# Kernel tuning notes

Measured on AMD Instinct MI355X. Metric: run time of the kernel, lower is better.

## Reference

```python
import jax, jax.numpy as jnp
import numpy as np

N = 50000      # nodes
E = 800000     # edges
P = 100000     # pos/neg candidate edges
IN = 128       # input feat dim
H, D = 2, 64   # heads, out_feats per head
HD = H * D     # 128
NEG_SLOPE = 0.2


def setup_inputs() -> dict:
    key = jax.random.key(0)
    ks = jax.random.split(key, 18)
    def gn(k, shape, fan_in):
        return jax.random.normal(k, shape, jnp.float32) * (1.0 / np.sqrt(fan_in))
    return {
        "x": jax.random.normal(ks[0], (N, IN), jnp.float32),
        "src": jax.random.randint(ks[1], (E,), 0, N),
        "dst": jax.random.randint(ks[2], (E,), 0, N),
        "pos_src": jax.random.randint(ks[3], (P,), 0, N),
        "pos_dst": jax.random.randint(ks[4], (P,), 0, N),
        "neg_src": jax.random.randint(ks[5], (P,), 0, N),
        "neg_dst": jax.random.randint(ks[6], (P,), 0, N),
        "W0": gn(ks[7], (IN, HD), IN),
        "attn0": gn(ks[8], (H, D), D),
        "W1": gn(ks[9], (HD, HD), HD),
        "attn1": gn(ks[10], (H, D), D),
        "Wp1": gn(ks[11], (HD, D), HD),
        "bp1": jnp.zeros((D,), jnp.float32),
        "Wp2": gn(ks[12], (D, D), D),
        "bp2": jnp.zeros((D,), jnp.float32),
        "Wp3": gn(ks[13], (D, 1), D),
        "bp3": jnp.zeros((1,), jnp.float32),
    }


def gatv2_layer(h, W, attn, src, dst, residual):
    # DGL GATv2Conv, share_weights=True, bias=False, feat_drop=attn_drop=0
    feat = (h @ W).reshape(N, H, D)            # [N,H,D]
    el = feat[src]                              # [E,H,D] gather at src
    er = feat[dst]                              # [E,H,D] gather at dst
    e = jax.nn.leaky_relu(el + er, NEG_SLOPE)   # [E,H,D]
    score = jnp.einsum('ehd,hd->eh', e, attn)   # [E,H]
    # edge softmax over incoming edges of each dst node
    m = jax.ops.segment_max(score, dst, num_segments=N)      # [N,H]
    p = jnp.exp(score - m[dst])                               # [E,H]
    s = jax.ops.segment_sum(p, dst, num_segments=N)           # [N,H]
    a = p / s[dst]                                             # [E,H]
    rst = jax.ops.segment_sum(el * a[:, :, None], dst, num_segments=N)  # [N,H,D]
    if residual:
        rst = rst + h.reshape(N, H, D)          # identity res_fc (dims match)
    return jax.nn.elu(rst).reshape(N, HD)       # flatten(1)


def reference(x, src, dst, pos_src, pos_dst, neg_src, neg_dst,
              W0, attn0, W1, attn1, Wp1, bp1, Wp2, bp2, Wp3, bp3):
    h = gatv2_layer(x, W0, attn0, src, dst, residual=False)
    h = gatv2_layer(h, W1, attn1, src, dst, residual=True)

    def predictor(z):
        z = jax.nn.relu(z @ Wp1 + bp1)
        z = jax.nn.relu(z @ Wp2 + bp2)
        return z @ Wp3 + bp3

    h_pos = predictor(h[pos_src] * h[pos_dst])  # [P,1]
    h_neg = predictor(h[neg_src] * h[neg_dst])  # [P,1]
    return (h_pos, h_neg)
```

## Files before the change

kernel.cpp:

```cpp
#include <hip/hip_runtime.h>
#include <math.h>

#define NN 50000
#define NE 800000
#define NP 100000
#define NEG_SLOPE 0.2f


__global__ void count_deg(const int* __restrict__ dst, int* __restrict__ cnt) {
    int i = blockIdx.x * blockDim.x + threadIdx.x;
    int st = gridDim.x * blockDim.x;
    for (; i < NE; i += st) atomicAdd(&cnt[dst[i]], 1);
}

__global__ __launch_bounds__(1024) void scan_deg(const int* __restrict__ cnt,
                                                 int* __restrict__ rowptr,
                                                 int* __restrict__ cursor) {
    __shared__ int wsum[16];
    __shared__ int carry;
    __shared__ int total;
    int tid = threadIdx.x;
    int lane = tid & 63, w = tid >> 6;
    if (tid == 0) carry = 0;
    __syncthreads();
    for (int base = 0; base < NN; base += 1024) {
        int idx = base + tid;
        int v = (idx < NN) ? cnt[idx] : 0;
        int x = v;
        #pragma unroll
        for (int mm = 1; mm < 64; mm <<= 1) {
            int y = __shfl_up(x, mm, 64);
            if (lane >= mm) x += y;
        }
        if (lane == 63) wsum[w] = x;
        __syncthreads();
        if (w == 0) {
            int orig = (lane < 16) ? wsum[lane] : 0;
            int t = orig;
            #pragma unroll
            for (int mm = 1; mm < 16; mm <<= 1) {
                int y = __shfl_up(t, mm, 64);
                if (lane >= mm) t += y;
            }
            if (lane < 16) wsum[lane] = t - orig;
            if (lane == 15) total = t;
        }
        __syncthreads();
        int excl = carry + wsum[w] + x - v;
        if (idx < NN) { rowptr[idx] = excl; cursor[idx] = excl; }
        __syncthreads();
        if (tid == 0) carry += total;
        __syncthreads();
    }
    if (tid == 0) rowptr[NN] = carry;
}

__global__ void scatter_edges(const int* __restrict__ src, const int* __restrict__ dst,
                              int* __restrict__ cursor, int* __restrict__ csrc) {
    int i = blockIdx.x * blockDim.x + threadIdx.x;
    int st = gridDim.x * blockDim.x;
    for (; i < NE; i += st) {
        int p = atomicAdd(&cursor[dst[i]], 1);
        csrc[p] = src[i];
    }
}


__global__ __launch_bounds__(256) void gemm128(const float* __restrict__ A,
                                               const float* __restrict__ W,
                                               float* __restrict__ out, int nrows) {
    __shared__ float Wt[128 * 132];
    __shared__ float rb[16 * 132];
    int tid = threadIdx.x;
    for (int idx = tid; idx < 128 * 128; idx += 256) {
        int k = idx >> 7, j = idx & 127;
        Wt[j * 132 + k] = W[idx];
    }
    __syncthreads();
    int lane = tid & 63, w = tid >> 6;
    int ntiles = (nrows + 15) >> 4;
    const float* w0p = &Wt[lane * 132];
    const float* w1p = &Wt[(64 + lane) * 132];
    for (int t = blockIdx.x; t < ntiles; t += gridDim.x) {
        int r0 = t << 4;
        for (int i = tid; i < 512; i += 256) {
            int rr = r0 + (i >> 5);
            float4 v = {0.f, 0.f, 0.f, 0.f};
            if (rr < nrows) v = ((const float4*)A)[(size_t)rr * 32 + (i & 31)];
            *(float4*)&rb[(i >> 5) * 132 + (i & 31) * 4] = v;
        }
        __syncthreads();
        float acc[4][2] = {};
        #pragma unroll 4
        for (int k4 = 0; k4 < 32; ++k4) {
            float4 wv0 = *(const float4*)&w0p[k4 * 4];
            float4 wv1 = *(const float4*)&w1p[k4 * 4];
            #pragma unroll
            for (int i2 = 0; i2 < 4; ++i2) {
                float4 av = *(const float4*)&rb[(w * 4 + i2) * 132 + k4 * 4];
                acc[i2][0] = fmaf(av.x, wv0.x, acc[i2][0]);
                acc[i2][0] = fmaf(av.y, wv0.y, acc[i2][0]);
                acc[i2][0] = fmaf(av.z, wv0.z, acc[i2][0]);
                acc[i2][0] = fmaf(av.w, wv0.w, acc[i2][0]);
                acc[i2][1] = fmaf(av.x, wv1.x, acc[i2][1]);
                acc[i2][1] = fmaf(av.y, wv1.y, acc[i2][1]);
                acc[i2][1] = fmaf(av.z, wv1.z, acc[i2][1]);
                acc[i2][1] = fmaf(av.w, wv1.w, acc[i2][1]);
            }
        }
        #pragma unroll
        for (int i2 = 0; i2 < 4; ++i2) {
            int rr = r0 + w * 4 + i2;
            if (rr < nrows) {
                out[(size_t)rr * 128 + lane]      = acc[i2][0];
                out[(size_t)rr * 128 + 64 + lane] = acc[i2][1];
            }
        }
        __syncthreads();
    }
}


__global__ void gat_fused(const float* __restrict__ feat,
                          const int* __restrict__ rowptr,
                          const int* __restrict__ csrc,
                          const float* __restrict__ attn,
                          const float* __restrict__ resid,
                          float* __restrict__ out) {
    int lane = threadIdx.x & 63;
    int wid = (blockIdx.x * blockDim.x + threadIdx.x) >> 6;
    int nw = (gridDim.x * blockDim.x) >> 6;
    int half = lane >> 5;
    int q = lane & 31;
    const float4* feat4 = (const float4*)feat;
    float4 at = ((const float4*)attn)[q];
    for (int d = wid; d < NN; d += nw) {
        int beg = rowptr[d], end = rowptr[d + 1];
        float4 fd = feat4[(size_t)d * 32 + q];
        float m = -INFINITY, s = 0.f;
        float ax = 0.f, ay = 0.f, az = 0.f, aw = 0.f;
        bool first = true;
        int i = beg + half;
        int sn = (i < end) ? csrc[i] : 0;
        float4 f = {0.f, 0.f, 0.f, 0.f};
        if (i < end) f = feat4[(size_t)sn * 32 + q];
        int snn = (i + 2 < end) ? csrc[i + 2] : 0;
        while (i < end) {
            float4 fn = {0.f, 0.f, 0.f, 0.f};
            if (i + 2 < end) fn = feat4[(size_t)snn * 32 + q];
            int sn2 = (i + 4 < end) ? csrc[i + 4] : 0;
            float ex = f.x + fd.x; ex = ex > 0.f ? ex : NEG_SLOPE * ex;
            float ey = f.y + fd.y; ey = ey > 0.f ? ey : NEG_SLOPE * ey;
            float ez = f.z + fd.z; ez = ez > 0.f ? ez : NEG_SLOPE * ez;
            float ew = f.w + fd.w; ew = ew > 0.f ? ew : NEG_SLOPE * ew;
            float part = ex * at.x + ey * at.y + ez * at.z + ew * at.w;
            part += __shfl_xor(part, 8, 64);
            part += __shfl_xor(part, 4, 64);
            part += __shfl_xor(part, 2, 64);
            part += __shfl_xor(part, 1, 64);
            float p = first ? 1.f : __expf(part - m);
            m = first ? part : m;
            first = false;
            s += p;
            ax = fmaf(f.x, p, ax);
            ay = fmaf(f.y, p, ay);
            az = fmaf(f.z, p, az);
            aw = fmaf(f.w, p, aw);
            f = fn; snn = sn2; i += 2;
        }
        float mo = __shfl_xor(m, 32, 64);
        float so = __shfl_xor(s, 32, 64);
        float ox = __shfl_xor(ax, 32, 64);
        float oy = __shfl_xor(ay, 32, 64);
        float oz = __shfl_xor(az, 32, 64);
        float ow = __shfl_xor(aw, 32, 64);
        float nm = fmaxf(m, mo);
        float sc0 = (m == nm) ? 1.f : __expf(m - nm);
        float sc1 = (mo == nm) ? 1.f : __expf(mo - nm);
        float S = s * sc0 + so * sc1;
        float inv = S > 0.f ? 1.f / S : 0.f;
        float vx = (ax * sc0 + ox * sc1) * inv;
        float vy = (ay * sc0 + oy * sc1) * inv;
        float vz = (az * sc0 + oz * sc1) * inv;
        float vw = (aw * sc0 + ow * sc1) * inv;
        if (resid) {
            float4 r = ((const float4*)resid)[(size_t)d * 32 + q];
            vx += r.x; vy += r.y; vz += r.z; vw += r.w;
        }
        vx = vx > 0.f ? vx : expm1f(vx);
        vy = vy > 0.f ? vy : expm1f(vy);
        vz = vz > 0.f ? vz : expm1f(vz);
        vw = vw > 0.f ? vw : expm1f(vw);
        if (half == 0) {
            float4 o; o.x = vx; o.y = vy; o.z = vz; o.w = vw;
            ((float4*)out)[(size_t)d * 32 + q] = o;
        }
    }
}


__global__ __launch_bounds__(256, 1) void predictor(const float* __restrict__ h,
                          const int* __restrict__ ps, const int* __restrict__ pd,
                          const int* __restrict__ ns, const int* __restrict__ nd,
                          const float* __restrict__ Wp1, const float* __restrict__ bp1,
                          const float* __restrict__ Wp2, const float* __restrict__ bp2,
                          const float* __restrict__ Wp3, const float* __restrict__ bp3,
                          float* __restrict__ out) {
    __shared__ float S[29696];
    int tid = threadIdx.x;
    for (int idx = tid; idx < 128 * 64; idx += 256) {
        int k = idx >> 6, c = idx & 63;
        S[c * 132 + k] = Wp1[idx];
    }
    for (int idx = tid; idx < 64 * 64; idx += 256) {
        int k = idx >> 6, c = idx & 63;
        S[8448 + c * 68 + k] = Wp2[idx];
    }
    __syncthreads();
    int lane = tid & 63;
    int w = tid >> 6;
    int cg = lane & 15, rg = lane >> 4;
    float* zz = S + 12800 + w * 4224;
    float b1v[4], b2v[4], w3v[4];
    #pragma unroll
    for (int i = 0; i < 4; ++i) {
        b1v[i] = bp1[cg + 16 * i];
        b2v[i] = bp2[cg + 16 * i];
        w3v[i] = Wp3[cg + 16 * i];
    }
    float b3 = bp3[0];
    int gw = blockIdx.x * 4 + w;
    int gnw = gridDim.x * 4;
    int ge = lane >> 1, gp = lane & 1;
    const float4* h4 = (const float4*)h;
    const int NT = (2 * NP) / 32;
    for (int T = gw; T < NT; T += gnw) {
        int e = T * 32 + ge;
        int a, b;
        if (e < NP) { a = ps[e]; b = pd[e]; }
        else        { a = ns[e - NP]; b = nd[e - NP]; }
        const float4* pa = h4 + (size_t)a * 32 + gp * 16;
        const float4* pb = h4 + (size_t)b * 32 + gp * 16;
        float* zrow = zz + ge * 132 + gp * 64;
        #pragma unroll
        for (int qq = 0; qq < 16; ++qq) {
            float4 va = pa[qq];
            float4 vb = pb[qq];
            float4 vz;
            vz.x = va.x * vb.x; vz.y = va.y * vb.y;
            vz.z = va.z * vb.z; vz.w = va.w * vb.w;
            *(float4*)&zrow[qq * 4] = vz;
        }
        float acc[8][4] = {};
        #pragma unroll 2
        for (int k4 = 0; k4 < 32; ++k4) {
            float4 wv[4];
            #pragma unroll
            for (int i = 0; i < 4; ++i)
                wv[i] = *(const float4*)&S[(cg + 16 * i) * 132 + k4 * 4];
            #pragma unroll
            for (int j = 0; j < 8; ++j) {
                float4 zv = *(const float4*)&zz[(rg * 8 + j) * 132 + k4 * 4];
                #pragma unroll
                for (int i = 0; i < 4; ++i) {
                    acc[j][i] = fmaf(zv.x, wv[i].x, acc[j][i]);
                    acc[j][i] = fmaf(zv.y, wv[i].y, acc[j][i]);
                    acc[j][i] = fmaf(zv.z, wv[i].z, acc[j][i]);
                    acc[j][i] = fmaf(zv.w, wv[i].w, acc[j][i]);
                }
            }
        }
        #pragma unroll
        for (int j = 0; j < 8; ++j) {
            #pragma unroll
            for (int i = 0; i < 4; ++i)
                zz[(rg * 8 + j) * 68 + cg + 16 * i] = fmaxf(acc[j][i] + b1v[i], 0.f);
        }
        float acc2[8][4] = {};
        #pragma unroll 2
        for (int k4 = 0; k4 < 16; ++k4) {
            float4 wv[4];
            #pragma unroll
            for (int i = 0; i < 4; ++i)
                wv[i] = *(const float4*)&S[8448 + (cg + 16 * i) * 68 + k4 * 4];
            #pragma unroll
            for (int j = 0; j < 8; ++j) {
                float4 zv = *(const float4*)&zz[(rg * 8 + j) * 68 + k4 * 4];
                #pragma unroll
                for (int i = 0; i < 4; ++i) {
                    acc2[j][i] = fmaf(zv.x, wv[i].x, acc2[j][i]);
                    acc2[j][i] = fmaf(zv.y, wv[i].y, acc2[j][i]);
                    acc2[j][i] = fmaf(zv.z, wv[i].z, acc2[j][i]);
                    acc2[j][i] = fmaf(zv.w, wv[i].w, acc2[j][i]);
                }
            }
        }
        float v[8];
        #pragma unroll
        for (int j = 0; j < 8; ++j) {
            float sv = 0.f;
            #pragma unroll
            for (int i = 0; i < 4; ++i)
                sv = fmaf(fmaxf(acc2[j][i] + b2v[i], 0.f), w3v[i], sv);
            v[j] = sv;
        }
        #pragma unroll
        for (int mm = 1; mm <= 8; mm <<= 1) {
            #pragma unroll
            for (int j = 0; j < 8; ++j) v[j] += __shfl_xor(v[j], mm, 64);
        }
        if (cg == 0) {
            float4 o0, o1;
            o0.x = v[0] + b3; o0.y = v[1] + b3; o0.z = v[2] + b3; o0.w = v[3] + b3;
            o1.x = v[4] + b3; o1.y = v[5] + b3; o1.z = v[6] + b3; o1.w = v[7] + b3;
            *(float4*)&out[T * 32 + rg * 8]     = o0;
            *(float4*)&out[T * 32 + rg * 8 + 4] = o1;
        }
    }
}

extern "C" void kernel_launch(void* const* d_in, const int* in_sizes, int n_in,
                              void* d_out, int out_size, void* d_ws, size_t ws_size,
                              hipStream_t stream) {
    const float* x       = (const float*)d_in[0];
    const int*   src     = (const int*)d_in[1];
    const int*   dst     = (const int*)d_in[2];
    const int*   pos_src = (const int*)d_in[3];
    const int*   pos_dst = (const int*)d_in[4];
    const int*   neg_src = (const int*)d_in[5];
    const int*   neg_dst = (const int*)d_in[6];
    const float* W0      = (const float*)d_in[7];
    const float* attn0   = (const float*)d_in[8];
    const float* W1      = (const float*)d_in[9];
    const float* attn1   = (const float*)d_in[10];
    const float* Wp1     = (const float*)d_in[11];
    const float* bp1     = (const float*)d_in[12];
    const float* Wp2     = (const float*)d_in[13];
    const float* bp2     = (const float*)d_in[14];
    const float* Wp3     = (const float*)d_in[15];
    const float* bp3     = (const float*)d_in[16];

    float* A = (float*)d_ws;
    float* B = A + (size_t)NN * 128;
    float* C = B + (size_t)NN * 128;
    int* cnt    = (int*)(C + (size_t)NN * 128);
    int* rowptr = cnt + NN;
    int* cursor = rowptr + NN + 1;
    int* csrc   = cursor + NN;
    float* out = (float*)d_out;

    hipMemsetAsync(cnt, 0, NN * sizeof(int), stream);
    count_deg<<<3125, 256, 0, stream>>>(dst, cnt);
    scan_deg<<<1, 1024, 0, stream>>>(cnt, rowptr, cursor);
    scatter_edges<<<3125, 256, 0, stream>>>(src, dst, cursor, csrc);

    gemm128<<<1024, 256, 0, stream>>>(x, W0, A, NN);
    gat_fused<<<3125, 256, 0, stream>>>(A, rowptr, csrc, attn0, nullptr, C);

    gemm128<<<1024, 256, 0, stream>>>(C, W1, A, NN);
    gat_fused<<<3125, 256, 0, stream>>>(A, rowptr, csrc, attn1, C, B);

    predictor<<<256, 256, 0, stream>>>(B, pos_src, pos_dst, neg_src, neg_dst,
                                       Wp1, bp1, Wp2, bp2, Wp3, bp3, out);
}
```

Before: 452.5 us.

## Swizzle LDS layouts, use DPP reductions, deepen gather prefetch, dynamic predictor tiles

```diff
diff --git a/kernel.cpp b/kernel.cpp
--- a/kernel.cpp
+++ b/kernel.cpp
@@ -5,6 +5,18 @@
 #define NE 800000
 #define NP 100000
 #define NEG_SLOPE 0.2f
+
+__device__ __forceinline__ float row_sum16(float v) {
+    int x = __float_as_int(v);
+    v += __int_as_float(__builtin_amdgcn_update_dpp(0, x, 0x128, 0xF, 0xF, true));
+    x = __float_as_int(v);
+    v += __int_as_float(__builtin_amdgcn_update_dpp(0, x, 0x124, 0xF, 0xF, true));
+    x = __float_as_int(v);
+    v += __int_as_float(__builtin_amdgcn_update_dpp(0, x, 0x4E, 0xF, 0xF, true));
+    x = __float_as_int(v);
+    v += __int_as_float(__builtin_amdgcn_update_dpp(0, x, 0xB1, 0xF, 0xF, true));
+    return v;
+}
 
 
 __global__ void count_deg(const int* __restrict__ dst, int* __restrict__ cnt) {
@@ -74,13 +86,14 @@
     int tid = threadIdx.x;
     for (int idx = tid; idx < 128 * 128; idx += 256) {
         int k = idx >> 7, j = idx & 127;
-        Wt[j * 132 + k] = W[idx];
+        Wt[j * 132 + ((((k >> 2) ^ ((j >> 3) & 7)) << 2) | (k & 3))] = W[idx];
     }
     __syncthreads();
     int lane = tid & 63, w = tid >> 6;
-    int ntiles = (nrows + 15) >> 4;
+    int wsw = ((lane >> 3) & 7) << 2;
     const float* w0p = &Wt[lane * 132];
     const float* w1p = &Wt[(64 + lane) * 132];
+    int ntiles = (nrows + 15) >> 4;
     for (int t = blockIdx.x; t < ntiles; t += gridDim.x) {
         int r0 = t << 4;
         for (int i = tid; i < 512; i += 256) {
@@ -93,11 +106,11 @@
         float acc[4][2] = {};
         #pragma unroll 4
         for (int k4 = 0; k4 < 32; ++k4) {
-            float4 wv0 = *(const float4*)&w0p[k4 * 4];
-            float4 wv1 = *(const float4*)&w1p[k4 * 4];
+            float4 wv0 = *(const float4*)&w0p[(k4 << 2) ^ wsw];
+            float4 wv1 = *(const float4*)&w1p[(k4 << 2) ^ wsw];
             #pragma unroll
             for (int i2 = 0; i2 < 4; ++i2) {
-                float4 av = *(const float4*)&rb[(w * 4 + i2) * 132 + k4 * 4];
+                float4 av = *(const float4*)&rb[(w * 4 + i2) * 132 + (k4 << 2)];
                 acc[i2][0] = fmaf(av.x, wv0.x, acc[i2][0]);
                 acc[i2][0] = fmaf(av.y, wv0.y, acc[i2][0]);
                 acc[i2][0] = fmaf(av.z, wv0.z, acc[i2][0]);
@@ -141,32 +154,29 @@
         float ax = 0.f, ay = 0.f, az = 0.f, aw = 0.f;
         bool first = true;
         int i = beg + half;
-        int sn = (i < end) ? csrc[i] : 0;
-        float4 f = {0.f, 0.f, 0.f, 0.f};
-        if (i < end) f = feat4[(size_t)sn * 32 + q];
-        int snn = (i + 2 < end) ? csrc[i + 2] : 0;
+        float4 f0 = {0.f, 0.f, 0.f, 0.f}, f1 = {0.f, 0.f, 0.f, 0.f};
+        if (i < end)     { int s0 = csrc[i];     f0 = feat4[(size_t)s0 * 32 + q]; }
+        if (i + 2 < end) { int s1 = csrc[i + 2]; f1 = feat4[(size_t)s1 * 32 + q]; }
+        int s2 = (i + 4 < end) ? csrc[i + 4] : 0;
         while (i < end) {
-            float4 fn = {0.f, 0.f, 0.f, 0.f};
-            if (i + 2 < end) fn = feat4[(size_t)snn * 32 + q];
-            int sn2 = (i + 4 < end) ? csrc[i + 4] : 0;
-            float ex = f.x + fd.x; ex = ex > 0.f ? ex : NEG_SLOPE * ex;
-            float ey = f.y + fd.y; ey = ey > 0.f ? ey : NEG_SLOPE * ey;
-            float ez = f.z + fd.z; ez = ez > 0.f ? ez : NEG_SLOPE * ez;
-            float ew = f.w + fd.w; ew = ew > 0.f ? ew : NEG_SLOPE * ew;
+            float4 f2 = {0.f, 0.f, 0.f, 0.f};
+            if (i + 4 < end) f2 = feat4[(size_t)s2 * 32 + q];
+            int s3 = (i + 6 < end) ? csrc[i + 6] : 0;
+            float ex = f0.x + fd.x; ex = ex > 0.f ? ex : NEG_SLOPE * ex;
+            float ey = f0.y + fd.y; ey = ey > 0.f ? ey : NEG_SLOPE * ey;
+            float ez = f0.z + fd.z; ez = ez > 0.f ? ez : NEG_SLOPE * ez;
+            float ew = f0.w + fd.w; ew = ew > 0.f ? ew : NEG_SLOPE * ew;
             float part = ex * at.x + ey * at.y + ez * at.z + ew * at.w;
-            part += __shfl_xor(part, 8, 64);
-            part += __shfl_xor(part, 4, 64);
-            part += __shfl_xor(part, 2, 64);
-            part += __shfl_xor(part, 1, 64);
+            part = row_sum16(part);
             float p = first ? 1.f : __expf(part - m);
             m = first ? part : m;
             first = false;
             s += p;
-            ax = fmaf(f.x, p, ax);
-            ay = fmaf(f.y, p, ay);
-            az = fmaf(f.z, p, az);
-            aw = fmaf(f.w, p, aw);
-            f = fn; snn = sn2; i += 2;
+            ax = fmaf(f0.x, p, ax);
+            ay = fmaf(f0.y, p, ay);
+            az = fmaf(f0.z, p, az);
+            aw = fmaf(f0.w, p, aw);
+            f0 = f1; f1 = f2; s2 = s3; i += 2;
         }
         float mo = __shfl_xor(m, 32, 64);
         float so = __shfl_xor(s, 32, 64);
@@ -199,20 +209,20 @@
 }
 
 
-__global__ __launch_bounds__(256, 1) void predictor(const float* __restrict__ h,
+__global__ __launch_bounds__(384, 1) void predictor(const float* __restrict__ h,
                           const int* __restrict__ ps, const int* __restrict__ pd,
                           const int* __restrict__ ns, const int* __restrict__ nd,
                           const float* __restrict__ Wp1, const float* __restrict__ bp1,
                           const float* __restrict__ Wp2, const float* __restrict__ bp2,
                           const float* __restrict__ Wp3, const float* __restrict__ bp3,
-                          float* __restrict__ out) {
-    __shared__ float S[29696];
+                          int* __restrict__ tilectr, float* __restrict__ out) {
+    __shared__ float S[38144];
     int tid = threadIdx.x;
-    for (int idx = tid; idx < 128 * 64; idx += 256) {
+    for (int idx = tid; idx < 128 * 64; idx += 384) {
         int k = idx >> 6, c = idx & 63;
         S[c * 132 + k] = Wp1[idx];
     }
-    for (int idx = tid; idx < 64 * 64; idx += 256) {
+    for (int idx = tid; idx < 64 * 64; idx += 384) {
         int k = idx >> 6, c = idx & 63;
         S[8448 + c * 68 + k] = Wp2[idx];
     }
@@ -220,6 +230,7 @@
     int lane = tid & 63;
     int w = tid >> 6;
     int cg = lane & 15, rg = lane >> 4;
+    int zsw = rg << 2;
     float* zz = S + 12800 + w * 4224;
     float b1v[4], b2v[4], w3v[4];
     #pragma unroll
@@ -229,19 +240,22 @@
         w3v[i] = Wp3[cg + 16 * i];
     }
     float b3 = bp3[0];
-    int gw = blockIdx.x * 4 + w;
-    int gnw = gridDim.x * 4;
     int ge = lane >> 1, gp = lane & 1;
+    int gsw = ((ge >> 3) & 3) << 2;
     const float4* h4 = (const float4*)h;
     const int NT = (2 * NP) / 32;
-    for (int T = gw; T < NT; T += gnw) {
+    int T = 0;
+    while (true) {
+        if (lane == 0) T = atomicAdd(tilectr, 1);
+        T = __shfl(T, 0, 64);
+        if (T >= NT) break;
         int e = T * 32 + ge;
         int a, b;
         if (e < NP) { a = ps[e]; b = pd[e]; }
         else        { a = ns[e - NP]; b = nd[e - NP]; }
         const float4* pa = h4 + (size_t)a * 32 + gp * 16;
         const float4* pb = h4 + (size_t)b * 32 + gp * 16;
-        float* zrow = zz + ge * 132 + gp * 64;
+        float* zrow = zz + ge * 132;
         #pragma unroll
         for (int qq = 0; qq < 16; ++qq) {
             float4 va = pa[qq];
@@ -249,7 +263,7 @@
             float4 vz;
             vz.x = va.x * vb.x; vz.y = va.y * vb.y;
             vz.z = va.z * vb.z; vz.w = va.w * vb.w;
-            *(float4*)&zrow[qq * 4] = vz;
+            *(float4*)&zrow[((((gp << 4) | qq) << 2) ^ gsw)] = vz;
         }
         float acc[8][4] = {};
         #pragma unroll 2
@@ -257,10 +271,10 @@
             float4 wv[4];
             #pragma unroll
             for (int i = 0; i < 4; ++i)
-                wv[i] = *(const float4*)&S[(cg + 16 * i) * 132 + k4 * 4];
+                wv[i] = *(const float4*)&S[(cg + 16 * i) * 132 + (k4 << 2)];
             #pragma unroll
             for (int j = 0; j < 8; ++j) {
-                float4 zv = *(const float4*)&zz[(rg * 8 + j) * 132 + k4 * 4];
+                float4 zv = *(const float4*)&zz[(rg * 8 + j) * 132 + ((k4 << 2) ^ zsw)];
                 #pragma unroll
                 for (int i = 0; i < 4; ++i) {
                     acc[j][i] = fmaf(zv.x, wv[i].x, acc[j][i]);
@@ -273,8 +287,11 @@
         #pragma unroll
         for (int j = 0; j < 8; ++j) {
             #pragma unroll
-            for (int i = 0; i < 4; ++i)
-                zz[(rg * 8 + j) * 68 + cg + 16 * i] = fmaxf(acc[j][i] + b1v[i], 0.f);
+            for (int i = 0; i < 4; ++i) {
+                int co = cg + 16 * i;
+                zz[(rg * 8 + j) * 68 + ((((co >> 2) ^ rg) << 2) | (co & 3))] =
+                    fmaxf(acc[j][i] + b1v[i], 0.f);
+            }
         }
         float acc2[8][4] = {};
         #pragma unroll 2
@@ -282,10 +299,10 @@
             float4 wv[4];
             #pragma unroll
             for (int i = 0; i < 4; ++i)
-                wv[i] = *(const float4*)&S[8448 + (cg + 16 * i) * 68 + k4 * 4];
+                wv[i] = *(const float4*)&S[8448 + (cg + 16 * i) * 68 + (k4 << 2)];
             #pragma unroll
             for (int j = 0; j < 8; ++j) {
-                float4 zv = *(const float4*)&zz[(rg * 8 + j) * 68 + k4 * 4];
+                float4 zv = *(const float4*)&zz[(rg * 8 + j) * 68 + ((k4 << 2) ^ zsw)];
                 #pragma unroll
                 for (int i = 0; i < 4; ++i) {
                     acc2[j][i] = fmaf(zv.x, wv[i].x, acc2[j][i]);
@@ -302,12 +319,7 @@
             #pragma unroll
             for (int i = 0; i < 4; ++i)
                 sv = fmaf(fmaxf(acc2[j][i] + b2v[i], 0.f), w3v[i], sv);
-            v[j] = sv;
-        }
-        #pragma unroll
-        for (int mm = 1; mm <= 8; mm <<= 1) {
-            #pragma unroll
-            for (int j = 0; j < 8; ++j) v[j] += __shfl_xor(v[j], mm, 64);
+            v[j] = row_sum16(sv);
         }
         if (cg == 0) {
             float4 o0, o1;
@@ -347,9 +359,11 @@
     int* rowptr = cnt + NN;
     int* cursor = rowptr + NN + 1;
     int* csrc   = cursor + NN;
+    int* tilectr = csrc + NE;
     float* out = (float*)d_out;
 
     hipMemsetAsync(cnt, 0, NN * sizeof(int), stream);
+    hipMemsetAsync(tilectr, 0, sizeof(int), stream);
     count_deg<<<3125, 256, 0, stream>>>(dst, cnt);
     scan_deg<<<1, 1024, 0, stream>>>(cnt, rowptr, cursor);
     scatter_edges<<<3125, 256, 0, stream>>>(src, dst, cursor, csrc);
@@ -360,6 +374,6 @@
     gemm128<<<1024, 256, 0, stream>>>(C, W1, A, NN);
     gat_fused<<<3125, 256, 0, stream>>>(A, rowptr, csrc, attn1, C, B);
 
-    predictor<<<256, 256, 0, stream>>>(B, pos_src, pos_dst, neg_src, neg_dst,
-                                       Wp1, bp1, Wp2, bp2, Wp3, bp3, out);
-}
+    predictor<<<256, 384, 0, stream>>>(B, pos_src, pos_dst, neg_src, neg_dst,
+                                       Wp1, bp1, Wp2, bp2, Wp3, bp3, tilectr, out);
+}
```

Result: slower. 478.4 us (+5.7%).
